# Optimization experiments

Measured on AMD Instinct MI355X. Metric: run time of the kernel, lower is better.

Reference implementation:

```python
import jax, jax.numpy as jnp
import numpy as np

INPUT_DIM = 1024
QUERY_DIM = 1024
KEY_DIM = 1024
VALUE_DIM = 1024


def setup_inputs() -> dict:
    key = jax.random.key(0)
    ks = jax.random.split(key, 7)
    B, N = 4, 2048
    s_in = 1.0 / np.sqrt(INPUT_DIM)
    return {
        "x": jax.random.normal(ks[0], (B, N, INPUT_DIM), dtype=jnp.float32),
        "Wq": jax.random.uniform(ks[1], (INPUT_DIM, QUERY_DIM), jnp.float32, -s_in, s_in),
        "bq": jax.random.uniform(ks[2], (QUERY_DIM,), jnp.float32, -s_in, s_in),
        "Wk": jax.random.uniform(ks[3], (INPUT_DIM, KEY_DIM), jnp.float32, -s_in, s_in),
        "bk": jax.random.uniform(ks[4], (KEY_DIM,), jnp.float32, -s_in, s_in),
        "Wv": jax.random.uniform(ks[5], (INPUT_DIM, VALUE_DIM), jnp.float32, -s_in, s_in),
        "bv": jax.random.uniform(ks[6], (VALUE_DIM,), jnp.float32, -s_in, s_in),
    }


def reference(x, Wq, bq, Wk, bk, Wv, bv):
    # projections: (B, N, D)
    q = jnp.einsum("bnd,de->bne", x, Wq) + bq
    k = jnp.einsum("bnd,de->bne", x, Wk) + bk
    v = jnp.einsum("bnd,de->bne", x, Wv) + bv
    scale = 1.0 / jnp.sqrt(jnp.float32(QUERY_DIM))
    scores = jnp.einsum("bqe,bke->bqk", q, k) * scale  # (B, N, N)
    attn = jax.nn.softmax(scores, axis=2)
    return jnp.einsum("bqk,bkv->bqv", attn, v)
```

## Files before the change

### kernel.cpp

```cpp
#include <hip/hip_runtime.h>
#include <hip/hip_bf16.h>

typedef __bf16 bf16x8 __attribute__((ext_vector_type(8)));
typedef float  f32x4  __attribute__((ext_vector_type(4)));

__device__ __forceinline__ void gload16(const __bf16* g, __bf16* l) {
  __builtin_amdgcn_global_load_lds(
      (const __attribute__((address_space(1))) void*)g,
      (__attribute__((address_space(3))) void*)l, 16, 0, 0);
}

__device__ __forceinline__ void stage_tile(const __bf16* __restrict__ g, int ld,
                                           __bf16* l, int wid, int lane) {
#pragma unroll
  for (int p = 0; p < 4; ++p) {
    int c    = p * 256 + wid * 64 + lane;
    int row  = c >> 3;
    int slog = (c & 7) ^ (row & 7);
    gload16(g + (long)row * ld + slog * 8,
            l + (p * 256 + wid * 64) * 8);
  }
}

__device__ __forceinline__ int lds_off(int r, int s) {
  return r * 128 + ((s * 16) ^ ((r & 7) << 4));
}

template <int OUTBF16, int BIASMODE, int DOSCALE>
__global__ __launch_bounds__(256, 2) void gemm_bt(
    const __bf16* __restrict__ A, const __bf16* __restrict__ Bt,
    const float* __restrict__ bias, void* __restrict__ Cv,
    int lda, int ldb, int ldc, int K,
    long sA, long sB, long sC, float scale) {
  __shared__ __bf16 lds[2][2][128 * 64];

  const int tid = threadIdx.x, wid = tid >> 6, lane = tid & 63;
  const int wr = wid >> 1, wc = wid & 1;
  const long brow = (long)blockIdx.y * 128;
  const long bcol = (long)blockIdx.x * 128;

  A  += (long)blockIdx.z * sA;
  Bt += (long)blockIdx.z * sB;

  const __bf16* ga = A + brow * lda;
  const __bf16* gb = Bt + bcol * ldb;
  const int nk = K >> 6;

  f32x4 zero = {0.f, 0.f, 0.f, 0.f};
  f32x4 acc[4][4];
#pragma unroll
  for (int m = 0; m < 4; ++m)
#pragma unroll
    for (int n = 0; n < 4; ++n) acc[m][n] = zero;

  stage_tile(ga, lda, &lds[0][0][0], wid, lane);
  stage_tile(gb, ldb, &lds[0][1][0], wid, lane);
  __syncthreads();

  for (int kt = 0; kt < nk; ++kt) {
    const int cur = kt & 1;
    if (kt + 1 < nk) {
      stage_tile(ga + (kt + 1) * 64, lda, &lds[cur ^ 1][0][0], wid, lane);
      stage_tile(gb + (kt + 1) * 64, ldb, &lds[cur ^ 1][1][0], wid, lane);
    }
    const char* Ab = (const char*)&lds[cur][0][0];
    const char* Bb = (const char*)&lds[cur][1][0];
#pragma unroll
    for (int ks = 0; ks < 2; ++ks) {
      bf16x8 af[4], bfr[4];
      const int s = ks * 4 + (lane >> 4);
#pragma unroll
      for (int m = 0; m < 4; ++m) {
        int r = wr * 64 + m * 16 + (lane & 15);
        af[m] = *(const bf16x8*)(Ab + lds_off(r, s));
      }
#pragma unroll
      for (int n = 0; n < 4; ++n) {
        int r = wc * 64 + n * 16 + (lane & 15);
        bfr[n] = *(const bf16x8*)(Bb + lds_off(r, s));
      }
#pragma unroll
      for (int m = 0; m < 4; ++m)
#pragma unroll
        for (int n = 0; n < 4; ++n)
          acc[m][n] = __builtin_amdgcn_mfma_f32_16x16x32_bf16(
              af[m], bfr[n], acc[m][n], 0, 0, 0);
    }
    __syncthreads();
  }

  const long cbase = (long)blockIdx.z * sC;
#pragma unroll
  for (int m = 0; m < 4; ++m) {
    const int row = (int)brow + wr * 64 + m * 16 + ((lane >> 4) << 2);
#pragma unroll
    for (int n = 0; n < 4; ++n) {
      const int col = (int)bcol + wc * 64 + n * 16 + (lane & 15);
#pragma unroll
      for (int r = 0; r < 4; ++r) {
        float v = acc[m][n][r];
        if (DOSCALE) v *= scale;
        if (BIASMODE == 1) v += bias[col];
        if (BIASMODE == 2) v += bias[row + r];
        if (OUTBF16)
          ((__bf16*)Cv)[cbase + (long)(row + r) * ldc + col] = (__bf16)v;
        else
          ((float*)Cv)[cbase + (long)(row + r) * ldc + col] = v;
      }
    }
  }
}

__global__ __launch_bounds__(256) void convert_x(const float* __restrict__ x,
                                                 __bf16* __restrict__ o) {
  const long i = ((long)blockIdx.x * 256 + threadIdx.x) * 8;
  float4 a = *(const float4*)(x + i);
  float4 b = *(const float4*)(x + i + 4);
  bf16x8 v;
  v[0] = (__bf16)a.x; v[1] = (__bf16)a.y; v[2] = (__bf16)a.z; v[3] = (__bf16)a.w;
  v[4] = (__bf16)b.x; v[5] = (__bf16)b.y; v[6] = (__bf16)b.z; v[7] = (__bf16)b.w;
  *(bf16x8*)(o + i) = v;
}

__global__ __launch_bounds__(256) void transpose_w(
    const float* __restrict__ W0, const float* __restrict__ W1,
    const float* __restrict__ W2, __bf16* __restrict__ T0,
    __bf16* __restrict__ T1, __bf16* __restrict__ T2) {
  const float* W = blockIdx.z == 0 ? W0 : (blockIdx.z == 1 ? W1 : W2);
  __bf16* T      = blockIdx.z == 0 ? T0 : (blockIdx.z == 1 ? T1 : T2);
  __shared__ float t[64][65];
  const int e0 = blockIdx.x * 64, d0 = blockIdx.y * 64;
  const int tr = threadIdx.x >> 2, tc = (threadIdx.x & 3) * 16;
  const float* src = W + (long)(d0 + tr) * 1024 + e0 + tc;
#pragma unroll
  for (int i = 0; i < 4; ++i) {
    float4 v = *(const float4*)(src + i * 4);
    t[tr][tc + i * 4 + 0] = v.x;
    t[tr][tc + i * 4 + 1] = v.y;
    t[tr][tc + i * 4 + 2] = v.z;
    t[tr][tc + i * 4 + 3] = v.w;
  }
  __syncthreads();
  __bf16* dst = T + (long)(e0 + tr) * 1024 + d0 + tc;
  bf16x8 v0, v1;
#pragma unroll
  for (int i = 0; i < 8; ++i) v0[i] = (__bf16)t[tc + i][tr];
#pragma unroll
  for (int i = 0; i < 8; ++i) v1[i] = (__bf16)t[tc + 8 + i][tr];
  *(bf16x8*)dst = v0;
  *(bf16x8*)(dst + 8) = v1;
}

__global__ __launch_bounds__(256) void softmax_rows(__bf16* __restrict__ P) {
  __bf16* p = P + (long)blockIdx.x * 2048;
  const int t = threadIdx.x, wid = t >> 6, lane = t & 63;
  bf16x8 v = *(bf16x8*)(p + t * 8);
  float f[8];
  float mx = -1e30f;
#pragma unroll
  for (int i = 0; i < 8; ++i) { f[i] = (float)v[i]; mx = fmaxf(mx, f[i]); }
#pragma unroll
  for (int o = 32; o > 0; o >>= 1) mx = fmaxf(mx, __shfl_xor(mx, o));
  __shared__ float redm[4], reds[4];
  if (lane == 0) redm[wid] = mx;
  __syncthreads();
  mx = fmaxf(fmaxf(redm[0], redm[1]), fmaxf(redm[2], redm[3]));
  float s = 0.f;
#pragma unroll
  for (int i = 0; i < 8; ++i) { f[i] = __expf(f[i] - mx); s += f[i]; }
#pragma unroll
  for (int o = 32; o > 0; o >>= 1) s += __shfl_xor(s, o);
  if (lane == 0) reds[wid] = s;
  __syncthreads();
  s = reds[0] + reds[1] + reds[2] + reds[3];
  const float inv = 1.0f / s;
#pragma unroll
  for (int i = 0; i < 8; ++i) v[i] = (__bf16)(f[i] * inv);
  *(bf16x8*)(p + t * 8) = v;
}

extern "C" void kernel_launch(void* const* d_in, const int* in_sizes, int n_in,
                              void* d_out, int out_size, void* d_ws,
                              size_t ws_size, hipStream_t stream) {
  const float* x  = (const float*)d_in[0];
  const float* Wq = (const float*)d_in[1];
  const float* bq = (const float*)d_in[2];
  const float* Wk = (const float*)d_in[3];
  const float* bk = (const float*)d_in[4];
  const float* Wv = (const float*)d_in[5];
  const float* bv = (const float*)d_in[6];
  float* out = (float*)d_out;

  char* ws = (char*)d_ws;
  __bf16* xb  = (__bf16*)(ws);
  __bf16* wqt = (__bf16*)(ws + (16l << 20));
  __bf16* wkt = (__bf16*)(ws + (18l << 20));
  __bf16* wvt = (__bf16*)(ws + (20l << 20));
  __bf16* q   = (__bf16*)(ws + (22l << 20));
  __bf16* kk  = (__bf16*)(ws + (38l << 20));
  __bf16* vt  = (__bf16*)(ws + (54l << 20));
  __bf16* S   = (__bf16*)(ws + (70l << 20));

  convert_x<<<4096, 256, 0, stream>>>(x, xb);
  transpose_w<<<dim3(16, 16, 3), 256, 0, stream>>>(Wq, Wk, Wv, wqt, wkt, wvt);

  gemm_bt<1, 1, 0><<<dim3(8, 64, 1), 256, 0, stream>>>(
      xb, wqt, bq, q, 1024, 1024, 1024, 1024, 0, 0, 0, 1.f);
  gemm_bt<1, 1, 0><<<dim3(8, 64, 1), 256, 0, stream>>>(
      xb, wkt, bk, kk, 1024, 1024, 1024, 1024, 0, 0, 0, 1.f);
  gemm_bt<1, 2, 0><<<dim3(64, 8, 1), 256, 0, stream>>>(
      wvt, xb, bv, vt, 1024, 1024, 8192, 1024, 0, 0, 0, 1.f);

  gemm_bt<1, 0, 1><<<dim3(16, 16, 4), 256, 0, stream>>>(
      q, kk, nullptr, S, 1024, 1024, 2048, 1024,
      2048l * 1024, 2048l * 1024, 2048l * 2048, 0.03125f);

  softmax_rows<<<8192, 256, 0, stream>>>(S);

  gemm_bt<0, 0, 0><<<dim3(8, 16, 4), 256, 0, stream>>>(
      S, vt, nullptr, out, 2048, 8192, 1024, 2048,
      2048l * 2048, 2048, 2048l * 1024, 1.f);
}
```

Measured before the change: 181.2 us.

## Restructure GEMM to 256x128 tiles with triple-buffered LDS pipeline and XCD remap

Replaces the 128x128 double-buffered GEMM with a 512-thread kernel that computes 256x128 tiles. It uses a three-stage LDS ring with explicit vmcnt waits, so global loads stay two tiles ahead of compute. It also remaps workgroup IDs so consecutive tiles land on the same XCD, and raises wave priority around the MFMA blocks. The aim is to hide global-load latency and improve L2 reuse, at the cost of 144KB of LDS per block, one block per CU, and fewer workgroups per launch.

New measurement: 208.6 us. +15.2%, slower.

```diff
diff --git a/kernel.cpp b/kernel.cpp
--- a/kernel.cpp
+++ b/kernel.cpp
@@ -10,15 +10,16 @@
       (__attribute__((address_space(3))) void*)l, 16, 0, 0);
 }
 
-__device__ __forceinline__ void stage_tile(const __bf16* __restrict__ g, int ld,
-                                           __bf16* l, int wid, int lane) {
-#pragma unroll
-  for (int p = 0; p < 4; ++p) {
-    int c    = p * 256 + wid * 64 + lane;
-    int row  = c >> 3;
-    int slog = (c & 7) ^ (row & 7);
-    gload16(g + (long)row * ld + slog * 8,
-            l + (p * 256 + wid * 64) * 8);
+template <int ROWS>
+__device__ __forceinline__ void stage(const __bf16* __restrict__ g, int ld,
+                                      __bf16* l, int wid, int lane) {
+#pragma unroll
+  for (int p = 0; p < ROWS / 64; ++p) {
+    int cbase = p * 512 + wid * 64;
+    int c     = cbase + lane;
+    int row   = c >> 3;
+    int slog  = (c & 7) ^ (row & 7);
+    gload16(g + (long)row * ld + slog * 8, l + cbase * 8);
   }
 }
 
@@ -27,75 +28,88 @@
 }
 
 template <int OUTBF16, int BIASMODE, int DOSCALE>
-__global__ __launch_bounds__(256, 2) void gemm_bt(
+__global__ __launch_bounds__(512, 1) void gemm_bt2(
     const __bf16* __restrict__ A, const __bf16* __restrict__ Bt,
     const float* __restrict__ bias, void* __restrict__ Cv,
     int lda, int ldb, int ldc, int K,
     long sA, long sB, long sC, float scale) {
-  __shared__ __bf16 lds[2][2][128 * 64];
+  __shared__ __align__(16) __bf16 ldsA[3][256 * 64];
+  __shared__ __align__(16) __bf16 ldsB[3][128 * 64];
 
   const int tid = threadIdx.x, wid = tid >> 6, lane = tid & 63;
-  const int wr = wid >> 1, wc = wid & 1;
-  const long brow = (long)blockIdx.y * 128;
-  const long bcol = (long)blockIdx.x * 128;
-
-  A  += (long)blockIdx.z * sA;
-  Bt += (long)blockIdx.z * sB;
-
-  const __bf16* ga = A + brow * lda;
-  const __bf16* gb = Bt + bcol * ldb;
+  const int wr = wid >> 2, wc = wid & 3;
+
+  const int gx = gridDim.x, gy = gridDim.y;
+  const int nwg = gx * gy * (int)gridDim.z;
+  int flat = ((int)blockIdx.z * gy + (int)blockIdx.y) * gx + (int)blockIdx.x;
+  flat = (flat & 7) * (nwg >> 3) + (flat >> 3);
+  const int bx = flat % gx;
+  const int by = (flat / gx) % gy;
+  const int bz = flat / (gx * gy);
+
+  const long brow = (long)by * 256;
+  const long bcol = (long)bx * 128;
+  const __bf16* ga = A + bz * sA + brow * lda;
+  const __bf16* gb = Bt + bz * sB + bcol * ldb;
   const int nk = K >> 6;
 
-  f32x4 zero = {0.f, 0.f, 0.f, 0.f};
-  f32x4 acc[4][4];
-#pragma unroll
-  for (int m = 0; m < 4; ++m)
-#pragma unroll
-    for (int n = 0; n < 4; ++n) acc[m][n] = zero;
-
-  stage_tile(ga, lda, &lds[0][0][0], wid, lane);
-  stage_tile(gb, ldb, &lds[0][1][0], wid, lane);
-  __syncthreads();
-
-  for (int kt = 0; kt < nk; ++kt) {
-    const int cur = kt & 1;
-    if (kt + 1 < nk) {
-      stage_tile(ga + (kt + 1) * 64, lda, &lds[cur ^ 1][0][0], wid, lane);
-      stage_tile(gb + (kt + 1) * 64, ldb, &lds[cur ^ 1][1][0], wid, lane);
+  f32x4 acc[8][2];
+#pragma unroll
+  for (int m = 0; m < 8; ++m)
+#pragma unroll
+    for (int n = 0; n < 2; ++n) acc[m][n] = (f32x4){0.f, 0.f, 0.f, 0.f};
+
+  stage<256>(ga, lda, ldsA[0], wid, lane);
+  stage<128>(gb, ldb, ldsB[0], wid, lane);
+  if (nk > 1) {
+    stage<256>(ga + 64, lda, ldsA[1], wid, lane);
+    stage<128>(gb + 64, ldb, ldsB[1], wid, lane);
+  }
+
+  for (int t = 0; t < nk; ++t) {
+    if (t > 0) asm volatile("s_barrier" ::: "memory");
+    if (t + 2 < nk) {
+      stage<256>(ga + (t + 2) * 64, lda, ldsA[(t + 2) % 3], wid, lane);
+      stage<128>(gb + (t + 2) * 64, ldb, ldsB[(t + 2) % 3], wid, lane);
     }
-    const char* Ab = (const char*)&lds[cur][0][0];
-    const char* Bb = (const char*)&lds[cur][1][0];
+    const int left = (nk - 1 - t) < 2 ? (nk - 1 - t) : 2;
+    if (left == 2)
+      asm volatile("s_waitcnt vmcnt(12)\n\ts_barrier" ::: "memory");
+    else if (left == 1)
+      asm volatile("s_waitcnt vmcnt(6)\n\ts_barrier" ::: "memory");
+    else
+      asm volatile("s_waitcnt vmcnt(0)\n\ts_barrier" ::: "memory");
+
+    const char* Ab = (const char*)ldsA[t % 3];
+    const char* Bb = (const char*)ldsB[t % 3];
 #pragma unroll
     for (int ks = 0; ks < 2; ++ks) {
-      bf16x8 af[4], bfr[4];
       const int s = ks * 4 + (lane >> 4);
-#pragma unroll
-      for (int m = 0; m < 4; ++m) {
-        int r = wr * 64 + m * 16 + (lane & 15);
-        af[m] = *(const bf16x8*)(Ab + lds_off(r, s));
-      }
-#pragma unroll
-      for (int n = 0; n < 4; ++n) {
-        int r = wc * 64 + n * 16 + (lane & 15);
-        bfr[n] = *(const bf16x8*)(Bb + lds_off(r, s));
-      }
-#pragma unroll
-      for (int m = 0; m < 4; ++m)
-#pragma unroll
-        for (int n = 0; n < 4; ++n)
+      bf16x8 af[8], bfr[2];
+#pragma unroll
+      for (int m = 0; m < 8; ++m)
+        af[m] = *(const bf16x8*)(Ab + lds_off(wr * 128 + m * 16 + (lane & 15), s));
+#pragma unroll
+      for (int n = 0; n < 2; ++n)
+        bfr[n] = *(const bf16x8*)(Bb + lds_off(wc * 32 + n * 16 + (lane & 15), s));
+      __builtin_amdgcn_s_setprio(1);
+#pragma unroll
+      for (int m = 0; m < 8; ++m)
+#pragma unroll
+        for (int n = 0; n < 2; ++n)
           acc[m][n] = __builtin_amdgcn_mfma_f32_16x16x32_bf16(
               af[m], bfr[n], acc[m][n], 0, 0, 0);
+      __builtin_amdgcn_s_setprio(0);
     }
-    __syncthreads();
-  }
-
-  const long cbase = (long)blockIdx.z * sC;
-#pragma unroll
-  for (int m = 0; m < 4; ++m) {
-    const int row = (int)brow + wr * 64 + m * 16 + ((lane >> 4) << 2);
-#pragma unroll
-    for (int n = 0; n < 4; ++n) {
-      const int col = (int)bcol + wc * 64 + n * 16 + (lane & 15);
+  }
+
+  const long cb = (long)bz * sC;
+#pragma unroll
+  for (int m = 0; m < 8; ++m) {
+    const int row = (int)brow + wr * 128 + m * 16 + ((lane >> 4) << 2);
+#pragma unroll
+    for (int n = 0; n < 2; ++n) {
+      const int col = (int)bcol + wc * 32 + n * 16 + (lane & 15);
 #pragma unroll
       for (int r = 0; r < 4; ++r) {
         float v = acc[m][n][r];
@@ -103,9 +117,9 @@
         if (BIASMODE == 1) v += bias[col];
         if (BIASMODE == 2) v += bias[row + r];
         if (OUTBF16)
-          ((__bf16*)Cv)[cbase + (long)(row + r) * ldc + col] = (__bf16)v;
+          ((__bf16*)Cv)[cb + (long)(row + r) * ldc + col] = (__bf16)v;
         else
-          ((float*)Cv)[cbase + (long)(row + r) * ldc + col] = v;
+          ((float*)Cv)[cb + (long)(row + r) * ldc + col] = v;
       }
     }
   }
@@ -204,20 +218,20 @@
   convert_x<<<4096, 256, 0, stream>>>(x, xb);
   transpose_w<<<dim3(16, 16, 3), 256, 0, stream>>>(Wq, Wk, Wv, wqt, wkt, wvt);
 
-  gemm_bt<1, 1, 0><<<dim3(8, 64, 1), 256, 0, stream>>>(
+  gemm_bt2<1, 1, 0><<<dim3(8, 32, 1), 512, 0, stream>>>(
       xb, wqt, bq, q, 1024, 1024, 1024, 1024, 0, 0, 0, 1.f);
-  gemm_bt<1, 1, 0><<<dim3(8, 64, 1), 256, 0, stream>>>(
+  gemm_bt2<1, 1, 0><<<dim3(8, 32, 1), 512, 0, stream>>>(
       xb, wkt, bk, kk, 1024, 1024, 1024, 1024, 0, 0, 0, 1.f);
-  gemm_bt<1, 2, 0><<<dim3(64, 8, 1), 256, 0, stream>>>(
+  gemm_bt2<1, 2, 0><<<dim3(64, 4, 1), 512, 0, stream>>>(
       wvt, xb, bv, vt, 1024, 1024, 8192, 1024, 0, 0, 0, 1.f);
 
-  gemm_bt<1, 0, 1><<<dim3(16, 16, 4), 256, 0, stream>>>(
+  gemm_bt2<1, 0, 1><<<dim3(16, 8, 4), 512, 0, stream>>>(
       q, kk, nullptr, S, 1024, 1024, 2048, 1024,
       2048l * 1024, 2048l * 1024, 2048l * 2048, 0.03125f);
 
   softmax_rows<<<8192, 256, 0, stream>>>(S);
 
-  gemm_bt<0, 0, 0><<<dim3(8, 16, 4), 256, 0, stream>>>(
+  gemm_bt2<0, 0, 0><<<dim3(8, 8, 4), 512, 0, stream>>>(
       S, vt, nullptr, out, 2048, 8192, 1024, 2048,
       2048l * 2048, 2048, 2048l * 1024, 1.f);
 }
```

## Fuse Q/K projections, remap workgroups for XCD locality, single-buffer LDS

Applied to the files above, without the earlier changes.

Q and K projections are merged into one GEMM over a concatenated transposed weight, writing interleaved QK output with a split bias lookup. Workgroup indices are remapped so consecutive tiles land on the same XCD, aiming for better L2 reuse. The double-buffered LDS prefetch is replaced by a single buffer with load-sync-compute, which shrinks LDS and may raise occupancy but loses load/compute overlap.

After: 193.9 us. 7.0% more time.

```diff
diff --git a/kernel.cpp b/kernel.cpp
--- a/kernel.cpp
+++ b/kernel.cpp
@@ -27,58 +27,53 @@
 }
 
 template <int OUTBF16, int BIASMODE, int DOSCALE>
-__global__ __launch_bounds__(256, 2) void gemm_bt(
+__global__ __launch_bounds__(256) void gemm6(
     const __bf16* __restrict__ A, const __bf16* __restrict__ Bt,
-    const float* __restrict__ bias, void* __restrict__ Cv,
-    int lda, int ldb, int ldc, int K,
+    const float* __restrict__ bias, const float* __restrict__ bias2,
+    void* __restrict__ Cv, int lda, int ldb, int ldc, int K,
     long sA, long sB, long sC, float scale) {
-  __shared__ __bf16 lds[2][2][128 * 64];
+  __shared__ __align__(16) __bf16 lA[128 * 64];
+  __shared__ __align__(16) __bf16 lB[128 * 64];
 
   const int tid = threadIdx.x, wid = tid >> 6, lane = tid & 63;
   const int wr = wid >> 1, wc = wid & 1;
-  const long brow = (long)blockIdx.y * 128;
-  const long bcol = (long)blockIdx.x * 128;
-
-  A  += (long)blockIdx.z * sA;
-  Bt += (long)blockIdx.z * sB;
-
-  const __bf16* ga = A + brow * lda;
-  const __bf16* gb = Bt + bcol * ldb;
+
+  const int gx = gridDim.x, gy = gridDim.y;
+  const int nwg = gx * gy * (int)gridDim.z;
+  int flat = ((int)blockIdx.z * gy + (int)blockIdx.y) * gx + (int)blockIdx.x;
+  flat = (flat & 7) * (nwg >> 3) + (flat >> 3);
+  const int bx = flat % gx;
+  const int by = (flat / gx) % gy;
+  const int bz = flat / (gx * gy);
+
+  const long brow = (long)by * 128;
+  const long bcol = (long)bx * 128;
+  const __bf16* ga = A + bz * sA + brow * lda;
+  const __bf16* gb = Bt + bz * sB + bcol * ldb;
   const int nk = K >> 6;
 
-  f32x4 zero = {0.f, 0.f, 0.f, 0.f};
   f32x4 acc[4][4];
 #pragma unroll
   for (int m = 0; m < 4; ++m)
 #pragma unroll
-    for (int n = 0; n < 4; ++n) acc[m][n] = zero;
-
-  stage_tile(ga, lda, &lds[0][0][0], wid, lane);
-  stage_tile(gb, ldb, &lds[0][1][0], wid, lane);
-  __syncthreads();
-
-  for (int kt = 0; kt < nk; ++kt) {
-    const int cur = kt & 1;
-    if (kt + 1 < nk) {
-      stage_tile(ga + (kt + 1) * 64, lda, &lds[cur ^ 1][0][0], wid, lane);
-      stage_tile(gb + (kt + 1) * 64, ldb, &lds[cur ^ 1][1][0], wid, lane);
-    }
-    const char* Ab = (const char*)&lds[cur][0][0];
-    const char* Bb = (const char*)&lds[cur][1][0];
+    for (int n = 0; n < 4; ++n) acc[m][n] = (f32x4){0.f, 0.f, 0.f, 0.f};
+
+  for (int t = 0; t < nk; ++t) {
+    stage_tile(ga + t * 64, lda, lA, wid, lane);
+    stage_tile(gb + t * 64, ldb, lB, wid, lane);
+    __syncthreads();
+    const char* Ab = (const char*)lA;
+    const char* Bb = (const char*)lB;
 #pragma unroll
     for (int ks = 0; ks < 2; ++ks) {
       bf16x8 af[4], bfr[4];
       const int s = ks * 4 + (lane >> 4);
 #pragma unroll
-      for (int m = 0; m < 4; ++m) {
-        int r = wr * 64 + m * 16 + (lane & 15);
-        af[m] = *(const bf16x8*)(Ab + lds_off(r, s));
-      }
-#pragma unroll
-      for (int n = 0; n < 4; ++n) {
-        int r = wc * 64 + n * 16 + (lane & 15);
-        bfr[n] = *(const bf16x8*)(Bb + lds_off(r, s));
-      }
+      for (int m = 0; m < 4; ++m)
+        af[m] = *(const bf16x8*)(Ab + lds_off(wr * 64 + m * 16 + (lane & 15), s));
+#pragma unroll
+      for (int n = 0; n < 4; ++n)
+        bfr[n] = *(const bf16x8*)(Bb + lds_off(wc * 64 + n * 16 + (lane & 15), s));
 #pragma unroll
       for (int m = 0; m < 4; ++m)
 #pragma unroll
@@ -89,7 +84,7 @@
     __syncthreads();
   }
 
-  const long cbase = (long)blockIdx.z * sC;
+  const long cb = (long)bz * sC;
 #pragma unroll
   for (int m = 0; m < 4; ++m) {
     const int row = (int)brow + wr * 64 + m * 16 + ((lane >> 4) << 2);
@@ -100,12 +95,12 @@
       for (int r = 0; r < 4; ++r) {
         float v = acc[m][n][r];
         if (DOSCALE) v *= scale;
-        if (BIASMODE == 1) v += bias[col];
+        if (BIASMODE == 1) v += (col < 1024) ? bias[col] : bias2[col - 1024];
         if (BIASMODE == 2) v += bias[row + r];
         if (OUTBF16)
-          ((__bf16*)Cv)[cbase + (long)(row + r) * ldc + col] = (__bf16)v;
+          ((__bf16*)Cv)[cb + (long)(row + r) * ldc + col] = (__bf16)v;
         else
-          ((float*)Cv)[cbase + (long)(row + r) * ldc + col] = v;
+          ((float*)Cv)[cb + (long)(row + r) * ldc + col] = v;
       }
     }
   }
@@ -192,32 +187,29 @@
   float* out = (float*)d_out;
 
   char* ws = (char*)d_ws;
-  __bf16* xb  = (__bf16*)(ws);
-  __bf16* wqt = (__bf16*)(ws + (16l << 20));
-  __bf16* wkt = (__bf16*)(ws + (18l << 20));
-  __bf16* wvt = (__bf16*)(ws + (20l << 20));
-  __bf16* q   = (__bf16*)(ws + (22l << 20));
-  __bf16* kk  = (__bf16*)(ws + (38l << 20));
-  __bf16* vt  = (__bf16*)(ws + (54l << 20));
-  __bf16* S   = (__bf16*)(ws + (70l << 20));
+  __bf16* xb   = (__bf16*)(ws);
+  __bf16* wqkt = (__bf16*)(ws + (16l << 20));
+  __bf16* wvt  = (__bf16*)(ws + (20l << 20));
+  __bf16* qk   = (__bf16*)(ws + (22l << 20));
+  __bf16* vt   = (__bf16*)(ws + (54l << 20));
+  __bf16* S    = (__bf16*)(ws + (70l << 20));
 
   convert_x<<<4096, 256, 0, stream>>>(x, xb);
-  transpose_w<<<dim3(16, 16, 3), 256, 0, stream>>>(Wq, Wk, Wv, wqt, wkt, wvt);
-
-  gemm_bt<1, 1, 0><<<dim3(8, 64, 1), 256, 0, stream>>>(
-      xb, wqt, bq, q, 1024, 1024, 1024, 1024, 0, 0, 0, 1.f);
-  gemm_bt<1, 1, 0><<<dim3(8, 64, 1), 256, 0, stream>>>(
-      xb, wkt, bk, kk, 1024, 1024, 1024, 1024, 0, 0, 0, 1.f);
-  gemm_bt<1, 2, 0><<<dim3(64, 8, 1), 256, 0, stream>>>(
-      wvt, xb, bv, vt, 1024, 1024, 8192, 1024, 0, 0, 0, 1.f);
-
-  gemm_bt<1, 0, 1><<<dim3(16, 16, 4), 256, 0, stream>>>(
-      q, kk, nullptr, S, 1024, 1024, 2048, 1024,
-      2048l * 1024, 2048l * 1024, 2048l * 2048, 0.03125f);
+  transpose_w<<<dim3(16, 16, 3), 256, 0, stream>>>(
+      Wq, Wk, Wv, wqkt, wqkt + 1024l * 1024, wvt);
+
+  gemm6<1, 1, 0><<<dim3(16, 64, 1), 256, 0, stream>>>(
+      xb, wqkt, bq, bk, qk, 1024, 1024, 2048, 1024, 0, 0, 0, 1.f);
+  gemm6<1, 2, 0><<<dim3(64, 8, 1), 256, 0, stream>>>(
+      wvt, xb, bv, nullptr, vt, 1024, 1024, 8192, 1024, 0, 0, 0, 1.f);
+
+  gemm6<1, 0, 1><<<dim3(16, 16, 4), 256, 0, stream>>>(
+      qk, qk + 1024, nullptr, nullptr, S, 2048, 2048, 2048, 1024,
+      2048l * 2048, 2048l * 2048, 2048l * 2048, 0.03125f);
 
   softmax_rows<<<8192, 256, 0, stream>>>(S);
 
-  gemm_bt<0, 0, 0><<<dim3(8, 16, 4), 256, 0, stream>>>(
-      S, vt, nullptr, out, 2048, 8192, 1024, 2048,
+  gemm6<0, 0, 0><<<dim3(8, 16, 4), 256, 0, stream>>>(
+      S, vt, nullptr, nullptr, out, 2048, 8192, 1024, 2048,
       2048l * 2048, 2048, 2048l * 1024, 1.f);
 }
```
